# Performance work log

Hardware: AMD Instinct MI355X
Metric: run time of the kernel (lower is better)

The kernel has to match this reference:

```python
import jax, jax.numpy as jnp
import numpy as np

N_NODES = 100_000
N_EDGES = 3_200_000
IN_DIM, HID, OUT_DIM = 500, 16, 500


def _gcn_conv(x, W, b, src, dst, norm, n_nodes):
    # PyG GCNConv: h = X W; out[dst] += norm * h[src]; out += b
    h = x @ W                                   # [N, out]
    msg = h[src] * norm[:, None]                # [E+N, out]
    out = jax.ops.segment_sum(msg, dst, num_segments=n_nodes)
    return out + b


def setup_inputs() -> dict:
    key = jax.random.key(0)
    ks = jax.random.split(key, 8)
    x = jax.random.normal(ks[0], (N_NODES, IN_DIM), dtype=jnp.float32)
    edge_index = jax.random.randint(ks[1], (2, N_EDGES), 0, N_NODES, dtype=jnp.int32)
    # Glorot-ish init scale for the linear weights
    W1 = jax.random.normal(ks[2], (IN_DIM, HID), dtype=jnp.float32) * (1.0 / np.sqrt(IN_DIM))
    b1 = jnp.zeros((HID,), dtype=jnp.float32)
    W2 = jax.random.normal(ks[3], (HID, HID), dtype=jnp.float32) * (1.0 / np.sqrt(HID))
    b2 = jnp.zeros((HID,), dtype=jnp.float32)
    W3 = jax.random.normal(ks[4], (HID, OUT_DIM), dtype=jnp.float32) * (1.0 / np.sqrt(HID))
    b3 = jnp.zeros((OUT_DIM,), dtype=jnp.float32)
    return {"x": x, "edge_index": edge_index, "W1": W1, "b1": b1,
            "W2": W2, "b2": b2, "W3": W3, "b3": b3}


def reference(x, edge_index, W1, b1, W2, b2, W3, b3):
    n = x.shape[0]
    loops = jnp.arange(n, dtype=edge_index.dtype)
    src = jnp.concatenate([edge_index[0], loops])  # add self-loops
    dst = jnp.concatenate([edge_index[1], loops])
    # symmetric normalization: deg over (A + I), norm_e = d^-1/2[src] * d^-1/2[dst]
    deg = jax.ops.segment_sum(jnp.ones_like(src, dtype=x.dtype), dst, num_segments=n)
    dis = jnp.where(deg > 0, jax.lax.rsqrt(deg), 0.0)
    norm = dis[src] * dis[dst]

    h = _gcn_conv(x, W1, b1, src, dst, norm, n)
    h = jax.nn.relu(h)
    h = _gcn_conv(h, W2, b2, src, dst, norm, n)
    h = jax.nn.relu(h)
    out = _gcn_conv(h, W3, b3, src, dst, norm, n)
    return out
```

## Files before the change

kernel.cpp:

```cpp
#include <hip/hip_runtime.h>

#define N_NODES 100000
#define N_EDGES 3200000
#define IN_DIM 500
#define HID 16
#define OUT_DIM 500

__global__ void k_deg(const int* __restrict__ dst, int* __restrict__ cnt, int E) {
    int e = blockIdx.x * blockDim.x + threadIdx.x;
    if (e < E) atomicAdd(&cnt[dst[e]], 1);
}

__global__ void k_dis(const int* __restrict__ cnt, float* __restrict__ dis, int n) {
    int i = blockIdx.x * blockDim.x + threadIdx.x;
    if (i < n) dis[i] = rsqrtf((float)(cnt[i] + 1));
}

__global__ __launch_bounds__(1024) void k_scanA(const int* __restrict__ cnt,
                                                int* __restrict__ rowptr,
                                                int* __restrict__ bsum) {
    __shared__ int sh[1024];
    int t = threadIdx.x;
    int i = blockIdx.x * 1024 + t;
    int v = (i < N_NODES) ? cnt[i] : 0;
    sh[t] = v;
    __syncthreads();
    for (int off = 1; off < 1024; off <<= 1) {
        int tmp = (t >= off) ? sh[t - off] : 0;
        __syncthreads();
        sh[t] += tmp;
        __syncthreads();
    }
    if (i < N_NODES) rowptr[i] = sh[t] - v;
    if (t == 1023) bsum[blockIdx.x] = sh[1023];
}

__global__ __launch_bounds__(128) void k_scanB(int* __restrict__ bsum, int nb) {
    __shared__ int sh[128];
    int t = threadIdx.x;
    int v = (t < nb) ? bsum[t] : 0;
    sh[t] = v;
    __syncthreads();
    for (int off = 1; off < 128; off <<= 1) {
        int tmp = (t >= off) ? sh[t - off] : 0;
        __syncthreads();
        sh[t] += tmp;
        __syncthreads();
    }
    if (t < nb) bsum[t] = sh[t] - v;
}

__global__ void k_scanC(int* __restrict__ rowptr, const int* __restrict__ bsum) {
    int i = blockIdx.x * blockDim.x + threadIdx.x;
    if (i < N_NODES) rowptr[i] += bsum[i >> 10];
    if (i == 0) rowptr[N_NODES] = N_EDGES;
}

__global__ void k_fill(const int* __restrict__ src, const int* __restrict__ dst,
                       const int* __restrict__ rowptr, int* __restrict__ cursor,
                       int* __restrict__ csr, int E) {
    int e = blockIdx.x * blockDim.x + threadIdx.x;
    if (e < E) {
        int d = dst[e];
        int p = rowptr[d] + atomicAdd(&cursor[d], 1);
        csr[p] = src[e];
    }
}

__global__ __launch_bounds__(256) void k_mm1(const float* __restrict__ x,
                                             const float* __restrict__ W,
                                             const float* __restrict__ dis,
                                             float* __restrict__ hp) {
    __shared__ float Ws[IN_DIM * HID];
    for (int t = threadIdx.x; t < IN_DIM * HID; t += 256) Ws[t] = W[t];
    __syncthreads();
    int i = blockIdx.x * 16 + (threadIdx.x >> 4);
    int j = threadIdx.x & 15;
    if (i >= N_NODES) return;
    const float4* xr = (const float4*)(x + (size_t)i * IN_DIM);
    float acc = 0.0f;
#pragma unroll 5
    for (int k4 = 0; k4 < IN_DIM / 4; ++k4) {
        float4 v = xr[k4];
        acc += v.x * Ws[(4 * k4 + 0) * HID + j];
        acc += v.y * Ws[(4 * k4 + 1) * HID + j];
        acc += v.z * Ws[(4 * k4 + 2) * HID + j];
        acc += v.w * Ws[(4 * k4 + 3) * HID + j];
    }
    hp[(size_t)i * HID + j] = dis[i] * acc;
}

__global__ __launch_bounds__(256) void k_mm2(const float* __restrict__ o,
                                             const float* __restrict__ W,
                                             const float* __restrict__ dis,
                                             float* __restrict__ hp) {
    __shared__ float Ws[HID * HID];
    if (threadIdx.x < HID * HID) Ws[threadIdx.x] = W[threadIdx.x];
    __syncthreads();
    int t = blockIdx.x * 256 + threadIdx.x;
    if (t >= N_NODES * HID) return;
    int i = t >> 4;
    int j = t & 15;
    const float* orow = o + (size_t)i * HID;
    float acc = 0.0f;
#pragma unroll
    for (int k = 0; k < HID; ++k) acc += orow[k] * Ws[k * HID + j];
    hp[t] = dis[i] * acc;
}

__global__ void k_scale(const float* __restrict__ o, const float* __restrict__ dis,
                        float* __restrict__ hp) {
    int t = blockIdx.x * blockDim.x + threadIdx.x;
    if (t < N_NODES * HID) hp[t] = dis[t >> 4] * o[t];
}

template <int RELU>
__global__ __launch_bounds__(256) void k_gather(const int* __restrict__ rowptr,
                                                const int* __restrict__ csr,
                                                const float* __restrict__ dis,
                                                const float* __restrict__ hp,
                                                const float* __restrict__ b,
                                                float* __restrict__ o) {
    int g = threadIdx.x >> 4;
    int f = threadIdx.x & 15;
    int d = blockIdx.x * 16 + g;
    int start = rowptr[d];
    int end = rowptr[d + 1];
    float s = 0.0f;
    for (int e0 = start; e0 < end; e0 += 16) {
        int idx = e0 + f;
        int sid = (idx < end) ? csr[idx] : 0;
        int m = end - e0;
        if (m > 16) m = 16;
        for (int j = 0; j < m; ++j) {
            int sj = __shfl(sid, j, 16);
            s += hp[(size_t)sj * HID + f];
        }
    }
    float di = dis[d];
    float v = di * (s + hp[(size_t)d * HID + f]);
    if (RELU) {
        v += b[f];
        v = v > 0.0f ? v : 0.0f;
    }
    o[(size_t)d * HID + f] = v;
}

__global__ __launch_bounds__(256) void k_mm3(const float* __restrict__ a,
                                             const float* __restrict__ W,
                                             const float* __restrict__ b,
                                             float* __restrict__ out) {
    __shared__ float Ws[HID * OUT_DIM];
    __shared__ float bs[OUT_DIM];
    for (int t = threadIdx.x; t < HID * OUT_DIM; t += 256) Ws[t] = W[t];
    for (int t = threadIdx.x; t < OUT_DIM; t += 256) bs[t] = b[t];
    __syncthreads();
    int ct = threadIdx.x & 127;
    int rt = threadIdx.x >> 7;
    int r0 = blockIdx.x * 8 + rt * 4;
    float areg[4][16];
#pragma unroll
    for (int rr = 0; rr < 4; ++rr) {
        const float4* ap = (const float4*)(a + (size_t)(r0 + rr) * HID);
        float4 v0 = ap[0], v1 = ap[1], v2 = ap[2], v3 = ap[3];
        areg[rr][0] = v0.x;  areg[rr][1] = v0.y;  areg[rr][2] = v0.z;  areg[rr][3] = v0.w;
        areg[rr][4] = v1.x;  areg[rr][5] = v1.y;  areg[rr][6] = v1.z;  areg[rr][7] = v1.w;
        areg[rr][8] = v2.x;  areg[rr][9] = v2.y;  areg[rr][10] = v2.z; areg[rr][11] = v2.w;
        areg[rr][12] = v3.x; areg[rr][13] = v3.y; areg[rr][14] = v3.z; areg[rr][15] = v3.w;
    }
    if (ct >= 125) return;
    int j0 = ct * 4;
    float acc[4][4];
#pragma unroll
    for (int rr = 0; rr < 4; ++rr) {
        acc[rr][0] = bs[j0];
        acc[rr][1] = bs[j0 + 1];
        acc[rr][2] = bs[j0 + 2];
        acc[rr][3] = bs[j0 + 3];
    }
#pragma unroll
    for (int k = 0; k < HID; ++k) {
        float4 w = *(const float4*)&Ws[k * OUT_DIM + j0];
#pragma unroll
        for (int rr = 0; rr < 4; ++rr) {
            acc[rr][0] += areg[rr][k] * w.x;
            acc[rr][1] += areg[rr][k] * w.y;
            acc[rr][2] += areg[rr][k] * w.z;
            acc[rr][3] += areg[rr][k] * w.w;
        }
    }
#pragma unroll
    for (int rr = 0; rr < 4; ++rr) {
        float4 r = make_float4(acc[rr][0], acc[rr][1], acc[rr][2], acc[rr][3]);
        *(float4*)&out[(size_t)(r0 + rr) * OUT_DIM + j0] = r;
    }
}

extern "C" void kernel_launch(void* const* d_in, const int* in_sizes, int n_in,
                              void* d_out, int out_size, void* d_ws, size_t ws_size,
                              hipStream_t stream) {
    const float* x  = (const float*)d_in[0];
    const int* ei   = (const int*)d_in[1];
    const float* W1 = (const float*)d_in[2];
    const float* b1 = (const float*)d_in[3];
    const float* W2 = (const float*)d_in[4];
    const float* b2 = (const float*)d_in[5];
    const float* W3 = (const float*)d_in[6];
    const float* b3 = (const float*)d_in[7];
    float* out = (float*)d_out;

    const int* src = ei;
    const int* dst = ei + N_EDGES;

    char* w = (char*)d_ws;
    float* dis    = (float*)(w);
    int*   cnt    = (int*)(w + 401408);
    int*   rowptr = (int*)(w + 802816);
    int*   bsum   = (int*)(w + 1205248);
    int*   csr    = (int*)(w + 1205760);
    float* hp     = (float*)(w + 14005760);
    float* o      = (float*)(w + 20405760);

    const int B = 256;
    int gN   = (N_NODES + B - 1) / B;
    int gE   = (N_EDGES + B - 1) / B;
    int gNH  = (N_NODES * HID + B - 1) / B;
    int gG   = N_NODES / 16;
    int gMM3 = N_NODES / 8;
    int gScanA = (N_NODES + 1023) / 1024;

    hipMemsetAsync(cnt, 0, N_NODES * sizeof(int), stream);
    k_deg<<<gE, B, 0, stream>>>(dst, cnt, N_EDGES);
    k_dis<<<gN, B, 0, stream>>>(cnt, dis, N_NODES);

    k_scanA<<<gScanA, 1024, 0, stream>>>(cnt, rowptr, bsum);
    k_scanB<<<1, 128, 0, stream>>>(bsum, gScanA);
    k_scanC<<<gN, B, 0, stream>>>(rowptr, bsum);
    hipMemsetAsync(cnt, 0, N_NODES * sizeof(int), stream);
    k_fill<<<gE, B, 0, stream>>>(src, dst, rowptr, cnt, csr, N_EDGES);

    k_mm1<<<(N_NODES + 15) / 16, B, 0, stream>>>(x, W1, dis, hp);
    k_gather<1><<<gG, B, 0, stream>>>(rowptr, csr, dis, hp, b1, o);

    k_mm2<<<gNH, B, 0, stream>>>(o, W2, dis, hp);
    k_gather<1><<<gG, B, 0, stream>>>(rowptr, csr, dis, hp, b2, o);

    k_scale<<<gNH, B, 0, stream>>>(o, dis, hp);
    k_gather<0><<<gG, B, 0, stream>>>(rowptr, csr, dis, hp, b3, o);
    k_mm3<<<gMM3, B, 0, stream>>>(o, W3, b3, out);
}
```

Baseline: 991.5 us.

## Use one wave per node in gather and two rows per thread in mm1

The gather kernel now assigns a full 64-lane wave to each destination node. Four 16-lane slots read different edges in parallel, and their partial sums are combined with xor shuffles. This replaces the serial per-edge loop that relied on broadcast shuffles and aims to raise memory-level parallelism on the irregular hp loads. The first matmul stores W transposed in shared memory so each thread can read float4 weight vectors, and each thread computes two node rows so every weight load is reused. In exchange, the gather launches four times as many blocks, and lanes in a wave sit idle on low-degree nodes.

```diff
diff --git a/kernel.cpp b/kernel.cpp
--- a/kernel.cpp
+++ b/kernel.cpp
@@ -71,23 +71,32 @@
                                              const float* __restrict__ W,
                                              const float* __restrict__ dis,
                                              float* __restrict__ hp) {
-    __shared__ float Ws[IN_DIM * HID];
-    for (int t = threadIdx.x; t < IN_DIM * HID; t += 256) Ws[t] = W[t];
-    __syncthreads();
-    int i = blockIdx.x * 16 + (threadIdx.x >> 4);
+    __shared__ float Wt[HID * IN_DIM];
+    for (int t = threadIdx.x; t < IN_DIM * HID; t += 256) {
+        int k = t >> 4;
+        int j = t & 15;
+        Wt[j * IN_DIM + k] = W[t];
+    }
+    __syncthreads();
+    int g = threadIdx.x >> 4;
     int j = threadIdx.x & 15;
-    if (i >= N_NODES) return;
-    const float4* xr = (const float4*)(x + (size_t)i * IN_DIM);
-    float acc = 0.0f;
+    int i0 = blockIdx.x * 32 + g;
+    int i1 = i0 + 16;
+    if (i1 >= N_NODES + 16) return;
+    const float4* xr0 = (const float4*)(x + (size_t)i0 * IN_DIM);
+    const float4* xr1 = (const float4*)(x + (size_t)i1 * IN_DIM);
+    const float4* wr = (const float4*)(Wt + j * IN_DIM);
+    float acc0 = 0.0f, acc1 = 0.0f;
 #pragma unroll 5
     for (int k4 = 0; k4 < IN_DIM / 4; ++k4) {
-        float4 v = xr[k4];
-        acc += v.x * Ws[(4 * k4 + 0) * HID + j];
-        acc += v.y * Ws[(4 * k4 + 1) * HID + j];
-        acc += v.z * Ws[(4 * k4 + 2) * HID + j];
-        acc += v.w * Ws[(4 * k4 + 3) * HID + j];
-    }
-    hp[(size_t)i * HID + j] = dis[i] * acc;
+        float4 w = wr[k4];
+        float4 a = xr0[k4];
+        float4 c = xr1[k4];
+        acc0 += a.x * w.x + a.y * w.y + a.z * w.z + a.w * w.w;
+        acc1 += c.x * w.x + c.y * w.y + c.z * w.z + c.w * w.w;
+    }
+    hp[(size_t)i0 * HID + j] = dis[i0] * acc0;
+    hp[(size_t)i1 * HID + j] = dis[i1] * acc1;
 }
 
 __global__ __launch_bounds__(256) void k_mm2(const float* __restrict__ o,
@@ -121,29 +130,28 @@
                                                 const float* __restrict__ hp,
                                                 const float* __restrict__ b,
                                                 float* __restrict__ o) {
-    int g = threadIdx.x >> 4;
-    int f = threadIdx.x & 15;
-    int d = blockIdx.x * 16 + g;
+    int wave = threadIdx.x >> 6;
+    int lane = threadIdx.x & 63;
+    int slot = lane >> 4;
+    int f = lane & 15;
+    int d = blockIdx.x * 4 + wave;
+    if (d >= N_NODES) return;
     int start = rowptr[d];
     int end = rowptr[d + 1];
     float s = 0.0f;
-    for (int e0 = start; e0 < end; e0 += 16) {
-        int idx = e0 + f;
-        int sid = (idx < end) ? csr[idx] : 0;
-        int m = end - e0;
-        if (m > 16) m = 16;
-        for (int j = 0; j < m; ++j) {
-            int sj = __shfl(sid, j, 16);
-            s += hp[(size_t)sj * HID + f];
-        }
-    }
+    for (int e = start + slot; e < end; e += 4) {
+        int sj = csr[e];
+        s += hp[(size_t)sj * HID + f];
+    }
+    s += __shfl_xor(s, 16);
+    s += __shfl_xor(s, 32);
     float di = dis[d];
     float v = di * (s + hp[(size_t)d * HID + f]);
     if (RELU) {
         v += b[f];
         v = v > 0.0f ? v : 0.0f;
     }
-    o[(size_t)d * HID + f] = v;
+    if (lane < 16) o[(size_t)d * HID + f] = v;
 }
 
 __global__ __launch_bounds__(256) void k_mm3(const float* __restrict__ a,
@@ -225,7 +233,8 @@
     int gN   = (N_NODES + B - 1) / B;
     int gE   = (N_EDGES + B - 1) / B;
     int gNH  = (N_NODES * HID + B - 1) / B;
-    int gG   = N_NODES / 16;
+    int gG   = (N_NODES + 3) / 4;
+    int gMM1 = N_NODES / 32;
     int gMM3 = N_NODES / 8;
     int gScanA = (N_NODES + 1023) / 1024;
 
@@ -239,7 +248,7 @@
     hipMemsetAsync(cnt, 0, N_NODES * sizeof(int), stream);
     k_fill<<<gE, B, 0, stream>>>(src, dst, rowptr, cnt, csr, N_EDGES);
 
-    k_mm1<<<(N_NODES + 15) / 16, B, 0, stream>>>(x, W1, dis, hp);
+    k_mm1<<<gMM1, B, 0, stream>>>(x, W1, dis, hp);
     k_gather<1><<<gG, B, 0, stream>>>(rowptr, csr, dis, hp, b1, o);
 
     k_mm2<<<gNH, B, 0, stream>>>(o, W2, dis, hp);
```

Result: slower. 1.062 ms (+7.1%).

## Compute full 16-wide output row per thread in the dense feature transforms

Applied to the files above, without the earlier changes.

k_mm1 and k_mm2 now give each thread one whole node row. Each thread holds 16 accumulators in registers, reads W directly from global memory with loads that are the same for every lane, and writes its results as float4. This drops the shared-memory staging of W and its __syncthreads, and it drops the 16-fold redundant reads of each x element. The cost is that adjacent lanes now read rows 2000 bytes apart, so x loads are not coalesced and depend on cache reuse. mm1 also runs far fewer blocks (about 391 instead of 6250), which lowers occupancy and latency hiding.

```diff
diff --git a/kernel.cpp b/kernel.cpp
--- a/kernel.cpp
+++ b/kernel.cpp
@@ -71,41 +71,57 @@
                                              const float* __restrict__ W,
                                              const float* __restrict__ dis,
                                              float* __restrict__ hp) {
-    __shared__ float Ws[IN_DIM * HID];
-    for (int t = threadIdx.x; t < IN_DIM * HID; t += 256) Ws[t] = W[t];
-    __syncthreads();
-    int i = blockIdx.x * 16 + (threadIdx.x >> 4);
-    int j = threadIdx.x & 15;
-    if (i >= N_NODES) return;
-    const float4* xr = (const float4*)(x + (size_t)i * IN_DIM);
-    float acc = 0.0f;
-#pragma unroll 5
+    int row = blockIdx.x * 256 + threadIdx.x;
+    if (row >= N_NODES) return;
+    const float4* xr = (const float4*)(x + (size_t)row * IN_DIM);
+    float acc[HID];
+#pragma unroll
+    for (int j = 0; j < HID; ++j) acc[j] = 0.0f;
     for (int k4 = 0; k4 < IN_DIM / 4; ++k4) {
-        float4 v = xr[k4];
-        acc += v.x * Ws[(4 * k4 + 0) * HID + j];
-        acc += v.y * Ws[(4 * k4 + 1) * HID + j];
-        acc += v.z * Ws[(4 * k4 + 2) * HID + j];
-        acc += v.w * Ws[(4 * k4 + 3) * HID + j];
-    }
-    hp[(size_t)i * HID + j] = dis[i] * acc;
+        float4 a = xr[k4];
+        const float* Wk = W + (size_t)(4 * k4) * HID;
+#pragma unroll
+        for (int j = 0; j < HID; ++j) {
+            acc[j] += a.x * Wk[j] + a.y * Wk[HID + j] +
+                      a.z * Wk[2 * HID + j] + a.w * Wk[3 * HID + j];
+        }
+    }
+    float di = dis[row];
+    float4* hr = (float4*)(hp + (size_t)row * HID);
+#pragma unroll
+    for (int q = 0; q < 4; ++q)
+        hr[q] = make_float4(di * acc[4 * q + 0], di * acc[4 * q + 1],
+                            di * acc[4 * q + 2], di * acc[4 * q + 3]);
 }
 
 __global__ __launch_bounds__(256) void k_mm2(const float* __restrict__ o,
                                              const float* __restrict__ W,
                                              const float* __restrict__ dis,
                                              float* __restrict__ hp) {
-    __shared__ float Ws[HID * HID];
-    if (threadIdx.x < HID * HID) Ws[threadIdx.x] = W[threadIdx.x];
-    __syncthreads();
-    int t = blockIdx.x * 256 + threadIdx.x;
-    if (t >= N_NODES * HID) return;
-    int i = t >> 4;
-    int j = t & 15;
-    const float* orow = o + (size_t)i * HID;
-    float acc = 0.0f;
-#pragma unroll
-    for (int k = 0; k < HID; ++k) acc += orow[k] * Ws[k * HID + j];
-    hp[t] = dis[i] * acc;
+    int row = blockIdx.x * 256 + threadIdx.x;
+    if (row >= N_NODES) return;
+    const float4* orow = (const float4*)(o + (size_t)row * HID);
+    float av[HID];
+#pragma unroll
+    for (int q = 0; q < 4; ++q) {
+        float4 a = orow[q];
+        av[4 * q + 0] = a.x; av[4 * q + 1] = a.y;
+        av[4 * q + 2] = a.z; av[4 * q + 3] = a.w;
+    }
+    float acc[HID];
+#pragma unroll
+    for (int j = 0; j < HID; ++j) acc[j] = 0.0f;
+#pragma unroll
+    for (int k = 0; k < HID; ++k) {
+#pragma unroll
+        for (int j = 0; j < HID; ++j) acc[j] += av[k] * W[k * HID + j];
+    }
+    float di = dis[row];
+    float4* hr = (float4*)(hp + (size_t)row * HID);
+#pragma unroll
+    for (int q = 0; q < 4; ++q)
+        hr[q] = make_float4(di * acc[4 * q + 0], di * acc[4 * q + 1],
+                            di * acc[4 * q + 2], di * acc[4 * q + 3]);
 }
 
 __global__ void k_scale(const float* __restrict__ o, const float* __restrict__ dis,
@@ -239,10 +255,10 @@
     hipMemsetAsync(cnt, 0, N_NODES * sizeof(int), stream);
     k_fill<<<gE, B, 0, stream>>>(src, dst, rowptr, cnt, csr, N_EDGES);
 
-    k_mm1<<<(N_NODES + 15) / 16, B, 0, stream>>>(x, W1, dis, hp);
+    k_mm1<<<gN, B, 0, stream>>>(x, W1, dis, hp);
     k_gather<1><<<gG, B, 0, stream>>>(rowptr, csr, dis, hp, b1, o);
 
-    k_mm2<<<gNH, B, 0, stream>>>(o, W2, dis, hp);
+    k_mm2<<<gN, B, 0, stream>>>(o, W2, dis, hp);
     k_gather<1><<<gG, B, 0, stream>>>(rowptr, csr, dis, hp, b2, o);
 
     k_scale<<<gNH, B, 0, stream>>>(o, dis, hp);
```

Result: no change. 986.6 us (-0.5%).
